# Optimization experiments

Hardware: AMD Instinct MI355X
Metric: run time of the kernel (lower is better)

## Reference

```python
import jax, jax.numpy as jnp
import numpy as np

N, L, S, E, A, D = 16, 256, 128, 128, 9, 768
ARG_ROLES = 23      # score width = ARG_ROLES + 1
MAX_ARG = 9         # hard-coded max_len_arg in the torch module
N_HID = 768


def setup_inputs() -> dict:
    key = jax.random.key(0)
    ks = jax.random.split(key, 10)
    all_embeddings = jax.random.normal(ks[0], (N, L, D), jnp.float32)
    # last-3-layer BERT attention maps, 12 heads, positive entries
    attn_last3 = jax.random.uniform(ks[1], (3, N, 12, L, L), jnp.float32)
    # per-sample sorted distinct first-subword indices (all positive, full length:
    # the ragged filter idxs>0 then keeps everything -> fixed-shape gather)
    idx_keys = jax.random.split(ks[2], N)
    cand = jnp.arange(1, L - MAX_ARG - 1)
    idxs_to_collect = jax.vmap(
        lambda k: jnp.sort(jax.random.choice(k, cand, (S + 2,), replace=False))
    )(idx_keys).astype(jnp.int32)
    is_triggers = (jax.random.uniform(ks[3], (N, S)) < 0.05).astype(jnp.float32)
    is_triggers = is_triggers.at[:, 0].set(1.0)  # >=1 trigger per sample
    entity_mapping = jax.random.normal(ks[4], (N, S, E), jnp.float32) * 0.05
    arg_weight_matrices = jax.random.normal(ks[5], (N, MAX_ARG, A), jnp.float32) * 0.3
    map_keys = jax.random.split(ks[6], N)
    arg_mapping = jax.vmap(
        lambda k: jax.random.permutation(k, ARG_ROLES + 1)[:A]
    )(map_keys).astype(jnp.int32)
    W1 = jax.random.normal(ks[7], (6 * D, N_HID), jnp.float32) * 0.02
    b1 = jnp.zeros((N_HID,), jnp.float32)
    W2 = jax.random.normal(ks[8], (N_HID, 1), jnp.float32) * 0.02
    b2 = jnp.zeros((1,), jnp.float32)
    return {
        "all_embeddings": all_embeddings,
        "attn_last3": attn_last3,
        "entity_mapping": entity_mapping,
        "arg_weight_matrices": arg_weight_matrices,
        "is_triggers": is_triggers,
        "W1": W1, "b1": b1, "W2": W2, "b2": b2,
        "idxs_to_collect": idxs_to_collect,
        "arg_mapping": arg_mapping,
    }


def reference(all_embeddings, attn_last3, entity_mapping, arg_weight_matrices,
              is_triggers, W1, b1, W2, b2, idxs_to_collect, arg_mapping):
    sqrt_d = jnp.sqrt(jnp.asarray(D, jnp.float32))
    sent_idx = idxs_to_collect[:, :S]                      # [N,S] first-subword ids
    # get_fist_subword_embeddings: ragged gather (full-length here)
    sent_emb = jnp.take_along_axis(all_embeddings, sent_idx[:, :, None], axis=1)  # [N,S,D]
    # arg-type tokens sit right after the second-to-last [SEP]
    arg_pos = idxs_to_collect[:, -2:-1] + 1 + jnp.arange(MAX_ARG)[None, :]        # [N,9]
    arg_raw = jnp.take_along_axis(all_embeddings, arg_pos[:, :, None], axis=1)    # [N,9,D]

    entity_emb = jnp.einsum('nsd,nse->ned', sent_emb, entity_mapping)             # [N,E,D]
    trig = jnp.sum(sent_emb * is_triggers[..., None], axis=1) \
           / jnp.sum(is_triggers, axis=1, keepdims=True)                          # [N,D]
    del trig  # _trigger is computed but unused downstream in the torch forward
    arg_emb = jnp.einsum('nkd,nka->nad', arg_raw, arg_weight_matrices)            # [N,A,D]

    # bi-attention scores (broadcast-mul-sum == contraction over D)
    t2a = jnp.einsum('ned,nad->nea', entity_emb, arg_emb) / sqrt_d
    w = (t2a - 5.0) / 2.0                                                         # [N,E,A]
    token_argAwared = jnp.einsum('nea,nad->ned', w, arg_emb)                      # [N,E,D]
    arg_tokenAwared = jnp.einsum('nea,ned->nad', w, entity_emb)                   # [N,A,D]

    # select_hidden_att for each of the last 3 layers
    att_mean = jnp.mean(attn_last3, axis=2)                                       # [3,N,L,L]
    def sel_layer(a):  # a: [N,L,L] -> row/col gather + row renorm
        s = jax.vmap(lambda m, i: m[i][:, i])(a, sent_idx)                        # [N,S,S]
        return s / (jnp.sum(s, axis=-1, keepdims=True) + 1e-9)
    t2t = (sel_layer(att_mean[0]) + sel_layer(att_mean[1]) + sel_layer(att_mean[2])) / 3.0

    h2h_sent = jnp.einsum('nst,ntd->nsd', t2t, sent_emb)                          # [N,S,D]
    # A_h2h and H_ are projected from sent space (S) to entity space (E)
    A_h2h_e = jnp.einsum('nsd,nse->ned', h2h_sent, entity_mapping)                # [N,E,D]
    H_e = entity_emb                                                              # sent_emb projected == entity_emb

    a2a = jax.nn.softmax(jnp.einsum('nad,nbd->nab', arg_emb, arg_emb), axis=-1)   # [N,A,A]
    u2u = jnp.einsum('nab,nbd->nad', a2a, arg_emb)                                # [N,A,D]

    shp = (N, E, A, D)
    H_    = jnp.broadcast_to(H_e[:, :, None, :], shp)
    U_    = jnp.broadcast_to(arg_emb[:, None, :, :], shp)
    A_h2u = jnp.broadcast_to(token_argAwared[:, :, None, :], shp)
    A_h2h = jnp.broadcast_to(A_h2h_e[:, :, None, :], shp)
    A_u2h = jnp.broadcast_to(arg_tokenAwared[:, None, :, :], shp)
    A_u2u = jnp.broadcast_to(u2u[:, None, :, :], shp)
    latent = jnp.concatenate([H_, U_, A_h2u, A_h2h, A_u2h, A_u2u], axis=-1)       # [N,E,A,6D]

    hid = jax.nn.gelu(latent @ W1 + b1, approximate=False)                        # [N,E,A,768]
    score = (hid @ W2 + b2)[..., 0]                                               # [N,E,A]

    # map_arg_to_ids: scatter each arg slot back to its global role id
    def scatter_one(s, ids):  # s [E,A], ids [A]
        return jnp.full((E, ARG_ROLES + 1), -1e6, jnp.float32).at[:, ids].set(s)
    new_score = jax.vmap(scatter_one)(score, arg_mapping)                         # [N,E,24]
    return new_score
```

## Files before the change

### kernel.cpp

```cpp
#include <hip/hip_runtime.h>
#include <math.h>

namespace {
constexpr int N_ = 16, L_ = 256, S_ = 128, E_ = 128, A_ = 9, D_ = 768, H_ = 768, RO_ = 24;
constexpr int IDXW = 130;
constexpr int W1R = 6 * D_;
constexpr float INV_SQRT_D = 0.03608439182435161f;
constexpr int PESZ = 2048 * 768;
constexpr int PASZ = 144 * 768;
constexpr int GB_GATHER = 0;
constexpr int GB_ENTMAP = 192;
constexpr int GB_W1T    = 208;
constexpr int GB_T2T    = 1072;
constexpr int GB_ARGU   = 2096;
constexpr int GB_TOTAL  = 2112;
}

using bshort8 = __attribute__((ext_vector_type(8))) short;
using f32x4v = __attribute__((ext_vector_type(4))) float;

__device__ __forceinline__ unsigned short f2bf(float f) {
    unsigned u = __builtin_bit_cast(unsigned, f);
    return (unsigned short)((u + 0x7fffu + ((u >> 16) & 1u)) >> 16);
}

__global__ __launch_bounds__(256) void stage1_k(const float* __restrict__ all_emb,
                                                const int* __restrict__ idxs,
                                                const float* __restrict__ ent_map,
                                                const float* __restrict__ W1,
                                                const float* __restrict__ argw,
                                                const float* __restrict__ attn,
                                                unsigned short* __restrict__ sentT,
                                                unsigned short* __restrict__ entmapT,
                                                short* __restrict__ W1t,
                                                unsigned short* __restrict__ t2tbf,
                                                float* __restrict__ argE,
                                                unsigned short* __restrict__ argEbf,
                                                unsigned short* __restrict__ u2ubf) {
    __shared__ __align__(16) unsigned char smem[33792];
    const int b = blockIdx.x, tid = threadIdx.x;

    if (b < GB_ENTMAP) {
        const int n = b / 12, d0 = (b % 12) * 64;
        auto tile = (unsigned short (*)[132])smem;
#pragma unroll
        for (int it = 0; it < 8; ++it) {
            const int lin = tid + 256 * it;
            const int s = lin >> 4, dq = (lin & 15) * 4;
            const int row = idxs[n * IDXW + s];
            const float4 v = *reinterpret_cast<const float4*>(all_emb + ((size_t)(n * L_ + row)) * D_ + d0 + dq);
            tile[dq + 0][s] = f2bf(v.x); tile[dq + 1][s] = f2bf(v.y);
            tile[dq + 2][s] = f2bf(v.z); tile[dq + 3][s] = f2bf(v.w);
        }
        __syncthreads();
#pragma unroll
        for (int it = 0; it < 8; ++it) {
            const int lin = tid + 256 * it;
            const int d = lin >> 5, s4 = (lin & 31) * 4;
            ushort4 v = {tile[d][s4], tile[d][s4 + 1], tile[d][s4 + 2], tile[d][s4 + 3]};
            *reinterpret_cast<ushort4*>(sentT + ((size_t)(n * D_) + d0 + d) * S_ + s4) = v;
        }
    } else if (b < GB_W1T) {
        const int n = b - GB_ENTMAP;
        auto tile = (unsigned short (*)[132])smem;
#pragma unroll
        for (int it = 0; it < 16; ++it) {
            const int lin = tid + 256 * it;
            const int s = lin >> 5, eq = (lin & 31) * 4;
            const float4 v = *reinterpret_cast<const float4*>(ent_map + ((size_t)(n * S_ + s)) * E_ + eq);
            tile[eq + 0][s] = f2bf(v.x); tile[eq + 1][s] = f2bf(v.y);
            tile[eq + 2][s] = f2bf(v.z); tile[eq + 3][s] = f2bf(v.w);
        }
        __syncthreads();
#pragma unroll
        for (int it = 0; it < 16; ++it) {
            const int lin = tid + 256 * it;
            const int e = lin >> 5, s4 = (lin & 31) * 4;
            ushort4 v = {tile[e][s4], tile[e][s4 + 1], tile[e][s4 + 2], tile[e][s4 + 3]};
            *reinterpret_cast<ushort4*>(entmapT + ((size_t)(n * E_) + e) * S_ + s4) = v;
        }
    } else if (b < GB_T2T) {
        const int b2 = b - GB_W1T;
        const int k0 = (b2 % 72) * 64, h0 = (b2 / 72) * 64;
        auto tile = (float (*)[65])smem;
        const int tx = tid & 63, ty = tid >> 6;
#pragma unroll
        for (int i = 0; i < 16; ++i) {
            const int r = ty + i * 4;
            tile[r][tx] = W1[(size_t)(k0 + r) * H_ + h0 + tx];
        }
        __syncthreads();
#pragma unroll
        for (int i = 0; i < 16; ++i) {
            const int r = ty + i * 4;
            W1t[(size_t)(h0 + r) * W1R + k0 + tx] = (short)f2bf(tile[tx][r]);
        }
    } else if (b < GB_ARGU) {
        const int idx = b - GB_T2T;
        const int n = idx >> 6;
        const int half = tid >> 7, t128 = tid & 127;
        const int s = ((idx & 63) << 1) | half;
        const int w = t128 >> 6, lane = tid & 63;
        float* sum2 = (float*)smem;
        float* part = (float*)(smem + 12288);
        const int is = idxs[n * IDXW + s], it = idxs[n * IDXW + t128];
#pragma unroll
        for (int l = 0; l < 3; ++l) {
            const float* base = attn + ((size_t)((l * N_ + n) * 12 + w * 6)) * (L_ * L_)
                              + (size_t)is * L_ + lane * 4;
            float4 acc = {0.f, 0.f, 0.f, 0.f};
#pragma unroll
            for (int h = 0; h < 6; ++h) {
// ... 2 lines not shown
            }
            *reinterpret_cast<float4*>(&sum2[(((half * 3 + l) * 2 + w) << 8) + lane * 4]) = acc;
        }
        __syncthreads();
        float m[3];
#pragma unroll
        for (int l = 0; l < 3; ++l) {
            m[l] = (sum2[(((half * 3 + l) * 2 + 0) << 8) + it] +
                    sum2[(((half * 3 + l) * 2 + 1) << 8) + it]) * (1.0f / 12.0f);
            float r = m[l];
#pragma unroll
            for (int off = 32; off; off >>= 1) r += __shfl_xor(r, off, 64);
            if (lane == 0) part[(half * 3 + l) * 2 + w] = r;
        }
        __syncthreads();
        float out = 0.f;
#pragma unroll
        for (int l = 0; l < 3; ++l)
            out += m[l] / (part[(half * 3 + l) * 2 + 0] + part[(half * 3 + l) * 2 + 1] + 1e-9f);
        t2tbf[((size_t)(n * S_ + s)) * S_ + t128] = f2bf(out * (1.0f / 3.0f));
    } else {
        const int n = b - GB_ARGU;
        auto wsm = (float (*)[A_])smem;
        auto part45 = (float (*)[4])(smem + 512);
        auto Psm = (float (*)[A_])(smem + 1536);
        if (tid < A_ * A_) wsm[tid / A_][tid % A_] = argw[n * A_ * A_ + tid];
        __syncthreads();
        const int p0 = idxs[n * IDXW + S_] + 1;
        float pp[45] = {};
        float vals[3][A_];
#pragma unroll
        for (int c = 0; c < 3; ++c) {
            const int d = tid + 256 * c;
            float raw[A_];
#pragma unroll
            for (int k = 0; k < A_; ++k) raw[k] = all_emb[((size_t)(n * L_ + p0 + k)) * D_ + d];
#pragma unroll
            for (int a = 0; a < A_; ++a) {
                float acc = 0.f;
#pragma unroll
                for (int k = 0; k < A_; ++k) acc = fmaf(raw[k], wsm[k][a], acc);
                vals[c][a] = acc;
                argE[((size_t)(n * A_ + a)) * D_ + d] = acc;
                argEbf[((size_t)(n * A_ + a)) * D_ + d] = f2bf(acc);
            }
            int p = 0;
#pragma unroll
            for (int a = 0; a < A_; ++a)
#pragma unroll
                for (int bb = a; bb < A_; ++bb) pp[p++] += vals[c][a] * vals[c][bb];
        }
        const int lane = tid & 63, wv = tid >> 6;
#pragma unroll
        for (int p = 0; p < 45; ++p) {
            float v = pp[p];
            for (int off = 32; off; off >>= 1) v += __shfl_down(v, off, 64);
            if (lane == 0) part45[p][wv] = v;
        }
        __syncthreads();
// ... 4 lines not shown
            float v[A_], mx = -1e30f;
#pragma unroll
            for (int bb = 0; bb < A_; ++bb) {
                const int lo = a < bb ? a : bb, hi = a < bb ? bb : a;
                v[bb] = part45[lo * (19 - lo) / 2 + hi - lo][0];
                mx = fmaxf(mx, v[bb]);
            }
            float sm = 0.f;
#pragma unroll
            for (int bb = 0; bb < A_; ++bb) { v[bb] = expf(v[bb] - mx); sm += v[bb]; }
            const float inv = 1.0f / sm;
#pragma unroll
            for (int bb = 0; bb < A_; ++bb) Psm[a][bb] = v[bb] * inv;
        }
        __syncthreads();
#pragma unroll
        for (int c = 0; c < 3; ++c) {
            const int d = tid + 256 * c;
#pragma unroll
            for (int a = 0; a < A_; ++a) {
                float acc = 0.f;
#pragma unroll
                for (int bb = 0; bb < A_; ++bb) acc = fmaf(Psm[a][bb], vals[c][bb], acc);
                u2ubf[((size_t)(n * A_ + a)) * D_ + d] = f2bf(acc);
            }
        }
    }
}

__global__ __launch_bounds__(256) void gemm_pair_k(const unsigned short* __restrict__ t2tbf,
                                                   const unsigned short* __restrict__ entmapT,
                                                   const unsigned short* __restrict__ sentT,
                                                   float* __restrict__ entf,
                                                   unsigned short* __restrict__ entbf,
                                                   unsigned short* __restrict__ h2hT) {
    __shared__ __align__(16) short As[128][40];
    __shared__ __align__(16) short Bs[64][40];
    const int n = blockIdx.y, c0 = blockIdx.x * 64, z = blockIdx.z;
    const unsigned short* A = (z == 0 ? t2tbf : entmapT) + (size_t)n * S_ * S_;
    const unsigned short* BT = sentT + (size_t)n * D_ * S_;
    const int tid = threadIdx.x;
    const int wave = tid >> 6, lane = tid & 63;
    const int row16 = lane & 15, quad = lane >> 4;
    f32x4v acc[2][4] = {};
    for (int k0 = 0; k0 < S_; k0 += 32) {
#pragma unroll
        for (int i = 0; i < 2; ++i) {
            const int idx = tid + 256 * i;
            const int r = idx >> 2, q = idx & 3;
            *reinterpret_cast<bshort8*>(&As[r][q * 8]) =
                *reinterpret_cast<const bshort8*>(A + (size_t)r * S_ + k0 + q * 8);
        }
        {
            const int col = tid >> 2, q = tid & 3;
            *reinterpret_cast<bshort8*>(&Bs[col][q * 8]) =
                *reinterpret_cast<const bshort8*>(BT + (size_t)(c0 + col) * S_ + k0 + q * 8);
        }
        __syncthreads();
        bshort8 a[2], b[4];
#pragma unroll
        for (int mi = 0; mi < 2; ++mi)
            a[mi] = *reinterpret_cast<const bshort8*>(&As[wave * 32 + mi * 16 + row16][quad * 8]);
#pragma unroll
        for (int ni = 0; ni < 4; ++ni)
            b[ni] = *reinterpret_cast<const bshort8*>(&Bs[ni * 16 + row16][quad * 8]);
#pragma unroll
        for (int mi = 0; mi < 2; ++mi)
#pragma unroll
            for (int ni = 0; ni < 4; ++ni)
                acc[mi][ni] = __builtin_amdgcn_mfma_f32_16x16x32_bf16(a[mi], b[ni], acc[mi][ni], 0, 0, 0);
        __syncthreads();
    }
#pragma unroll
    for (int mi = 0; mi < 2; ++mi) {
#pragma unroll
        for (int ni = 0; ni < 4; ++ni) {
            const int rbase = wave * 32 + mi * 16 + quad * 4;
            const int col = c0 + ni * 16 + row16;
            if (z == 0) {
                ushort4 v = {f2bf(acc[mi][ni][0]), f2bf(acc[mi][ni][1]),
                             f2bf(acc[mi][ni][2]), f2bf(acc[mi][ni][3])};
                *reinterpret_cast<ushort4*>(h2hT + (size_t)n * D_ * S_ + (size_t)col * S_ + rbase) = v;
            } else {
#pragma unroll
                for (int t = 0; t < 4; ++t) {
                    const size_t o = ((size_t)n * S_ + rbase + t) * D_ + col;
                    entf[o] = acc[mi][ni][t];
                    entbf[o] = f2bf(acc[mi][ni][t]);
                }
            }
        }
    }
}

__global__ __launch_bounds__(256) void gemm2_k(const unsigned short* __restrict__ entmapT,
                                               const unsigned short* __restrict__ h2hT,
                                               const unsigned short* __restrict__ entbf,
                                               const unsigned short* __restrict__ argEbf,
                                               unsigned short* __restrict__ Ah2hbf,
                                               float* __restrict__ wbuf) {
    const int bx = blockIdx.x, tid = threadIdx.x;
    const int wave = tid >> 6, lane = tid & 63;
    const int row16 = lane & 15, quad = lane >> 4;
    if (bx < 192) {
        __shared__ __align__(16) short As[128][40];
        __shared__ __align__(16) short Bs[64][40];
        const int n = bx / 12, c0 = (bx % 12) * 64;
        const unsigned short* A = entmapT + (size_t)n * S_ * S_;
        const unsigned short* BT = h2hT + (size_t)n * D_ * S_;
        f32x4v acc[2][4] = {};
        for (int k0 = 0; k0 < S_; k0 += 32) {
#pragma unroll
            for (int i = 0; i < 2; ++i) {
                const int idx = tid + 256 * i;
                const int r = idx >> 2, q = idx & 3;
                *reinterpret_cast<bshort8*>(&As[r][q * 8]) =
                    *reinterpret_cast<const bshort8*>(A + (size_t)r * S_ + k0 + q * 8);
            }
            {
                const int col = tid >> 2, q = tid & 3;
                *reinterpret_cast<bshort8*>(&Bs[col][q * 8]) =
                    *reinterpret_cast<const bshort8*>(BT + (size_t)(c0 + col) * S_ + k0 + q * 8);
            }
            __syncthreads();
            bshort8 a[2], b[4];
#pragma unroll
            for (int mi = 0; mi < 2; ++mi)
                a[mi] = *reinterpret_cast<const bshort8*>(&As[wave * 32 + mi * 16 + row16][quad * 8]);
#pragma unroll
            for (int ni = 0; ni < 4; ++ni)
                b[ni] = *reinterpret_cast<const bshort8*>(&Bs[ni * 16 + row16][quad * 8]);
#pragma unroll
            for (int mi = 0; mi < 2; ++mi)
#pragma unroll
                for (int ni = 0; ni < 4; ++ni)
                    acc[mi][ni] = __builtin_amdgcn_mfma_f32_16x16x32_bf16(a[mi], b[ni], acc[mi][ni], 0, 0, 0);
            __syncthreads();
        }
#pragma unroll
        for (int mi = 0; mi < 2; ++mi)
#pragma unroll
            for (int ni = 0; ni < 4; ++ni) {
                const int rbase = wave * 32 + mi * 16 + quad * 4;
                const int col = c0 + ni * 16 + row16;
#pragma unroll
                for (int t = 0; t < 4; ++t)
                    Ah2hbf[((size_t)n * S_ + rbase + t) * D_ + col] = f2bf(acc[mi][ni][t]);
            }
    } else {
        const int n = bx - 192;
        const unsigned short* Aent = entbf + (size_t)n * E_ * D_;
        const unsigned short* Barg = argEbf + (size_t)n * A_ * D_;
        f32x4v acc[2] = {};
        for (int k0 = 0; k0 < D_; k0 += 32) {
            bshort8 a[2], b;
#pragma unroll
            for (int mi = 0; mi < 2; ++mi)
                a[mi] = *reinterpret_cast<const bshort8*>(Aent + (size_t)(wave * 32 + mi * 16 + row16) * D_ + k0 + quad * 8);
            b = *reinterpret_cast<const bshort8*>(Barg + (size_t)row16 * D_ + k0 + quad * 8);
#pragma unroll
            for (int mi = 0; mi < 2; ++mi)
                acc[mi] = __builtin_amdgcn_mfma_f32_16x16x32_bf16(a[mi], b, acc[mi], 0, 0, 0);
        }
        if (row16 < A_) {
#pragma unroll
            for (int mi = 0; mi < 2; ++mi)
#pragma unroll
                for (int t = 0; t < 4; ++t) {
                    const int e = wave * 32 + mi * 16 + quad * 4 + t;
                    const float w = (acc[mi][t] * INV_SQRT_D - 5.0f) * 0.5f;
                    wbuf[((size_t)(n * E_ + e)) * A_ + row16] = w;
                }
        }
    }
}

__global__ __launch_bounds__(256) void post_k(const float* __restrict__ wbuf,
                                              const float* __restrict__ argE,
                                              const float* __restrict__ entf,
                                              unsigned short* __restrict__ tokAbf,
                                              unsigned short* __restrict__ argTbf) {
    const int b = blockIdx.x, tid = threadIdx.x;
    if (b < N_ * E_) {
        const int n = b >> 7, e = b & 127;
        __shared__ float wl[A_];
        if (tid < A_) wl[tid] = wbuf[(size_t)(n * E_ + e) * A_ + tid];
        __syncthreads();
        const float* ar = argE + (size_t)n * A_ * D_;
#pragma unroll
        for (int c = 0; c < 3; ++c) {
            const int d = tid + 256 * c;
            float s = 0.f;
#pragma unroll
            for (int a = 0; a < A_; ++a) s = fmaf(wl[a], ar[(size_t)a * D_ + d], s);
            tokAbf[((size_t)(n * E_ + e)) * D_ + d] = f2bf(s);
        }
    } else {
        const int idx = b - N_ * E_;
        const int n = idx / A_, a = idx % A_;
        __shared__ float wl[E_];
        if (tid < E_) wl[tid] = wbuf[(size_t)(n * E_ + tid) * A_ + a];
        __syncthreads();
        const float* eb = entf + (size_t)n * E_ * D_;
#pragma unroll
        for (int c = 0; c < 3; ++c) {
            const int d = tid + 256 * c;
            float acc = 0.f;
            for (int e = 0; e < E_; ++e) acc = fmaf(wl[e], eb[(size_t)e * D_ + d], acc);
            argTbf[((size_t)(n * A_ + a)) * D_ + d] = f2bf(acc);
        }
    }
}

__global__ __launch_bounds__(256) void mfma_mlp_k(const unsigned short* __restrict__ e0,
                                                  const unsigned short* __restrict__ e1,
                                                  const unsigned short* __restrict__ e2,
                                                  const unsigned short* __restrict__ a0,
                                                  const unsigned short* __restrict__ a1,
                                                  const unsigned short* __restrict__ a2,
                                                  const short* __restrict__ W1t,
                                                  float* __restrict__ Pe3, float* __restrict__ Pa3) {
    __shared__ __align__(16) short As[128][40];
    __shared__ __align__(16) short Bs[64][40];
    const int bx = blockIdx.x;
    const int seg = bx % 3;
    const int blk = bx / 3;
    const bool isPa = blk >= 16;
    const unsigned short* Aseg;
    int woff;
    if (isPa) {
        Aseg = seg == 0 ? a0 : (seg == 1 ? a1 : a2);
        woff = seg == 0 ? 1 * D_ : (seg == 1 ? 4 * D_ : 5 * D_);
    } else {
        Aseg = seg == 0 ? e0 : (seg == 1 ? e1 : e2);
        woff = seg == 0 ? 0 : (seg == 1 ? 2 * D_ : 3 * D_);
    }
    const int M = isPa ? N_ * A_ : N_ * E_;
    const int r0 = (isPa ? blk - 16 : blk) * 128;
    float* C = isPa ? (Pa3 + (size_t)seg * PASZ) : (Pe3 + (size_t)seg * PESZ);
    const int c0 = blockIdx.y * 64;
    const int tid = threadIdx.x;
    const int wave = tid >> 6, lane = tid & 63;
    const int row16 = lane & 15, quad = lane >> 4;
    f32x4v acc[2][4] = {};
    for (int kk = 0; kk < D_; kk += 32) {
#pragma unroll
        for (int i = 0; i < 2; ++i) {
            const int idx = tid + 256 * i;
            const int r = idx >> 2, q = idx & 3;
            bshort8 av = {};
            if (r0 + r < M) av = *reinterpret_cast<const bshort8*>(Aseg + (size_t)(r0 + r) * D_ + kk + q * 8);
            *reinterpret_cast<bshort8*>(&As[r][q * 8]) = av;
        }
        {
            const int col = tid >> 2, q = tid & 3;
            *reinterpret_cast<bshort8*>(&Bs[col][q * 8]) =
                *reinterpret_cast<const bshort8*>(W1t + (size_t)(c0 + col) * W1R + woff + kk + q * 8);
        }
        __syncthreads();
        bshort8 a[2], b[4];
#pragma unroll
        for (int mi = 0; mi < 2; ++mi)
            a[mi] = *reinterpret_cast<const bshort8*>(&As[wave * 32 + mi * 16 + row16][quad * 8]);
#pragma unroll
        for (int ni = 0; ni < 4; ++ni)
            b[ni] = *reinterpret_cast<const bshort8*>(&Bs[ni * 16 + row16][quad * 8]);
#pragma unroll
        for (int mi = 0; mi < 2; ++mi)
#pragma unroll
            for (int ni = 0; ni < 4; ++ni)
                acc[mi][ni] = __builtin_amdgcn_mfma_f32_16x16x32_bf16(a[mi], b[ni], acc[mi][ni], 0, 0, 0);
        __syncthreads();
    }
#pragma unroll
    for (int mi = 0; mi < 2; ++mi) {
#pragma unroll
        for (int ni = 0; ni < 4; ++ni) {
            const int rbase = r0 + wave * 32 + mi * 16 + quad * 4;
            const int col = c0 + ni * 16 + row16;
#pragma unroll
            for (int t = 0; t < 4; ++t)
                if (rbase + t < M) C[(size_t)(rbase + t) * H_ + col] = acc[mi][ni][t];
        }
    }
}

__global__ __launch_bounds__(256) void score_k(const float* __restrict__ Pe3, const float* __restrict__ Pa3,
                                               const float* __restrict__ b1, const float* __restrict__ W2,
                                               const float* __restrict__ b2, const int* __restrict__ arg_map,
                                               float* __restrict__ out) {
    const int n = blockIdx.x >> 7, e = blockIdx.x & 127;
    const int tid = threadIdx.x;
    __shared__ float paS[A_ * H_];
    __shared__ float part[A_][4];
    float* orow = out + ((size_t)(n * E_ + e)) * RO_;
    if (tid < RO_) orow[tid] = -1000000.0f;
    for (int i = tid; i < A_ * H_; i += 256) {
        const size_t o = (size_t)n * A_ * H_ + i;
        paS[i] = Pa3[o] + Pa3[PASZ + o] + Pa3[2 * PASZ + o];
    }
    __syncthreads();
    const size_t ro = ((size_t)(n * E_ + e)) * H_;
    float acc[A_] = {};
    for (int h = tid; h < H_; h += 256) {
        const float pe = Pe3[ro + h] + Pe3[PESZ + ro + h] + Pe3[2 * PESZ + ro + h] + b1[h];
        const float w2 = W2[h];
#pragma unroll
        for (int a = 0; a < A_; ++a) {
            const float x = pe + paS[a * H_ + h];
            const float g = x * 0.5f * (1.0f + erff(x * 0.70710678118654752f));
            acc[a] = fmaf(g, w2, acc[a]);
        }
    }
    const int lane = tid & 63, wv = tid >> 6;
#pragma unroll
    for (int a = 0; a < A_; ++a)
        for (int off = 32; off; off >>= 1) acc[a] += __shfl_down(acc[a], off, 64);
    if (lane == 0)
        for (int a = 0; a < A_; ++a) part[a][wv] = acc[a];
    __syncthreads();
// ... 7 lines not shown
                              void* d_out, int out_size, void* d_ws, size_t ws_size,
                              hipStream_t stream) {
    const float* all_emb = (const float*)d_in[0];
    const float* attn    = (const float*)d_in[1];
    const float* ent_map = (const float*)d_in[2];
    const float* argw    = (const float*)d_in[3];
    const float* W1 = (const float*)d_in[5];
    const float* b1 = (const float*)d_in[6];
    const float* W2 = (const float*)d_in[7];
    const float* b2 = (const float*)d_in[8];
    const int* idxs    = (const int*)d_in[9];
    const int* arg_map = (const int*)d_in[10];
    float* out = (float*)d_out;

    float* ws = (float*)d_ws;
    float* entf = ws + 0;
    float* Pe3  = ws + 1572864;
    float* argE = ws + 6291456;
    float* wbuf = ws + 6402048;
    float* Pa3  = ws + 6420480;
    short*          W1t     = (short*)(ws + 6752256);
    unsigned short* sentT   = (unsigned short*)(ws + 8521728);
    unsigned short* entmapT = (unsigned short*)(ws + 9308160);
    unsigned short* t2tbf   = (unsigned short*)(ws + 9439232);
    unsigned short* argEbf  = (unsigned short*)(ws + 9570304);
    unsigned short* u2ubf   = (unsigned short*)(ws + 9625600);
    unsigned short* entbf   = (unsigned short*)(ws + 9680896);
    unsigned short* h2hT    = (unsigned short*)(ws + 10467328);
    unsigned short* Ah2hbf  = (unsigned short*)(ws + 11253760);
    unsigned short* tokAbf  = (unsigned short*)(ws + 12040192);
    unsigned short* argTbf  = (unsigned short*)(ws + 12826624);

    stage1_k<<<GB_TOTAL, 256, 0, stream>>>(all_emb, idxs, ent_map, W1, argw, attn,
                                           sentT, entmapT, W1t, t2tbf, argE, argEbf, u2ubf);

    gemm_pair_k<<<dim3(D_ / 64, N_, 2), 256, 0, stream>>>(t2tbf, entmapT, sentT, entf, entbf, h2hT);

    gemm2_k<<<208, 256, 0, stream>>>(entmapT, h2hT, entbf, argEbf, Ah2hbf, wbuf);

    post_k<<<N_ * E_ + N_ * A_, 256, 0, stream>>>(wbuf, argE, entf, tokAbf, argTbf);

    mfma_mlp_k<<<dim3(54, H_ / 64), 256, 0, stream>>>(entbf, tokAbf, Ah2hbf, argEbf, argTbf, u2ubf, W1t, Pe3, Pa3);

    score_k<<<N_ * E_, 256, 0, stream>>>(Pe3, Pa3, b1, W2, b2, arg_map, out);

    (void)in_sizes; (void)n_in; (void)out_size; (void)ws_size;
}
```

Before: 318.2 us.

## Reassociate MLP first layer through W1 to shrink the GEMM chain

Restructures the pipeline so the embedding gather is multiplied by W1 slices first, and the entity, attention and softmax mixing matrices are then applied to the already projected 768-wide products. The separate entity, h2h, token-aware and u2u intermediates and their split-K partial outputs go away, and the six-kernel chain becomes five kernels with fused partial sums. The aim is to cut GEMM work and intermediate memory traffic. In exchange, more bf16 rounding points sit in a different order, and the kernels have more complex block-index dispatch.

```diff
diff --git a/kernel.cpp b/kernel.cpp
--- a/kernel.cpp
+++ b/kernel.cpp
@@ -6,14 +6,12 @@
 constexpr int IDXW = 130;
 constexpr int W1R = 6 * D_;
 constexpr float INV_SQRT_D = 0.03608439182435161f;
-constexpr int PESZ = 2048 * 768;
-constexpr int PASZ = 144 * 768;
-constexpr int GB_GATHER = 0;
-constexpr int GB_ENTMAP = 192;
-constexpr int GB_W1T    = 208;
-constexpr int GB_T2T    = 1072;
-constexpr int GB_ARGU   = 2096;
-constexpr int GB_TOTAL  = 2112;
+constexpr int GB_T2T    = 0;
+constexpr int GB_W1T    = 1024;
+constexpr int GB_GATHER = 1888;
+constexpr int GB_ENTMAP = 1952;
+constexpr int GB_ARGU   = 1968;
+constexpr int GB_TOTAL  = 1984;
 }
 
 using bshort8 = __attribute__((ext_vector_type(8))) short;
@@ -22,6 +20,46 @@
 __device__ __forceinline__ unsigned short f2bf(float f) {
     unsigned u = __builtin_bit_cast(unsigned, f);
     return (unsigned short)((u + 0x7fffu + ((u >> 16) & 1u)) >> 16);
+}
+__device__ __forceinline__ float bf2f(unsigned short u) {
+    return __builtin_bit_cast(float, ((unsigned)u) << 16);
+}
+
+__device__ __forceinline__ void gemm_tileK(const unsigned short* __restrict__ A, int lda,
+                                           const unsigned short* __restrict__ BT, int ldb,
+                                           int klen, int c0, int tid,
+                                           short (*As)[40], short (*Bs)[40],
+                                           f32x4v acc[2][4]) {
+    const int wave = tid >> 6, lane = tid & 63;
+    const int row16 = lane & 15, quad = lane >> 4;
+    for (int k0 = 0; k0 < klen; k0 += 32) {
+#pragma unroll
+        for (int i = 0; i < 2; ++i) {
+            const int idx = tid + 256 * i;
+            const int r = idx >> 2, q = idx & 3;
+            *reinterpret_cast<bshort8*>(&As[r][q * 8]) =
+                *reinterpret_cast<const bshort8*>(A + (size_t)r * lda + k0 + q * 8);
+        }
+        {
+            const int col = tid >> 2, q = tid & 3;
+            *reinterpret_cast<bshort8*>(&Bs[col][q * 8]) =
+                *reinterpret_cast<const bshort8*>(BT + (size_t)(c0 + col) * ldb + k0 + q * 8);
+        }
+        __syncthreads();
+        bshort8 a[2], b[4];
+#pragma unroll
+        for (int mi = 0; mi < 2; ++mi)
+            a[mi] = *reinterpret_cast<const bshort8*>(&As[wave * 32 + mi * 16 + row16][quad * 8]);
+#pragma unroll
+        for (int ni = 0; ni < 4; ++ni)
+            b[ni] = *reinterpret_cast<const bshort8*>(&Bs[ni * 16 + row16][quad * 8]);
+#pragma unroll
+        for (int mi = 0; mi < 2; ++mi)
+#pragma unroll
+            for (int ni = 0; ni < 4; ++ni)
+                acc[mi][ni] = __builtin_amdgcn_mfma_f32_16x16x32_bf16(a[mi], b[ni], acc[mi][ni], 0, 0, 0);
+        __syncthreads();
+    }
 }
 
 __global__ __launch_bounds__(256) void stage1_k(const float* __restrict__ all_emb,
@@ -30,72 +68,16 @@
                                                 const float* __restrict__ W1,
                                                 const float* __restrict__ argw,
                                                 const float* __restrict__ attn,
-                                                unsigned short* __restrict__ sentT,
+                                                unsigned short* __restrict__ sentbf,
                                                 unsigned short* __restrict__ entmapT,
                                                 short* __restrict__ W1t,
                                                 unsigned short* __restrict__ t2tbf,
-                                                float* __restrict__ argE,
                                                 unsigned short* __restrict__ argEbf,
-                                                unsigned short* __restrict__ u2ubf) {
+                                                float* __restrict__ Pmat) {
     __shared__ __align__(16) unsigned char smem[33792];
     const int b = blockIdx.x, tid = threadIdx.x;
 
-    if (b < GB_ENTMAP) {
-        const int n = b / 12, d0 = (b % 12) * 64;
-        auto tile = (unsigned short (*)[132])smem;
-#pragma unroll
-        for (int it = 0; it < 8; ++it) {
-            const int lin = tid + 256 * it;
-            const int s = lin >> 4, dq = (lin & 15) * 4;
-            const int row = idxs[n * IDXW + s];
-            const float4 v = *reinterpret_cast<const float4*>(all_emb + ((size_t)(n * L_ + row)) * D_ + d0 + dq);
-            tile[dq + 0][s] = f2bf(v.x); tile[dq + 1][s] = f2bf(v.y);
-            tile[dq + 2][s] = f2bf(v.z); tile[dq + 3][s] = f2bf(v.w);
-        }
-        __syncthreads();
-#pragma unroll
-        for (int it = 0; it < 8; ++it) {
-            const int lin = tid + 256 * it;
-            const int d = lin >> 5, s4 = (lin & 31) * 4;
-            ushort4 v = {tile[d][s4], tile[d][s4 + 1], tile[d][s4 + 2], tile[d][s4 + 3]};
-            *reinterpret_cast<ushort4*>(sentT + ((size_t)(n * D_) + d0 + d) * S_ + s4) = v;
-        }
-    } else if (b < GB_W1T) {
-        const int n = b - GB_ENTMAP;
-        auto tile = (unsigned short (*)[132])smem;
-#pragma unroll
-        for (int it = 0; it < 16; ++it) {
-            const int lin = tid + 256 * it;
-            const int s = lin >> 5, eq = (lin & 31) * 4;
-            const float4 v = *reinterpret_cast<const float4*>(ent_map + ((size_t)(n * S_ + s)) * E_ + eq);
-            tile[eq + 0][s] = f2bf(v.x); tile[eq + 1][s] = f2bf(v.y);
-            tile[eq + 2][s] = f2bf(v.z); tile[eq + 3][s] = f2bf(v.w);
-        }
-        __syncthreads();
-#pragma unroll
-        for (int it = 0; it < 16; ++it) {
-            const int lin = tid + 256 * it;
-            const int e = lin >> 5, s4 = (lin & 31) * 4;
-            ushort4 v = {tile[e][s4], tile[e][s4 + 1], tile[e][s4 + 2], tile[e][s4 + 3]};
-            *reinterpret_cast<ushort4*>(entmapT + ((size_t)(n * E_) + e) * S_ + s4) = v;
-        }
-    } else if (b < GB_T2T) {
-        const int b2 = b - GB_W1T;
-        const int k0 = (b2 % 72) * 64, h0 = (b2 / 72) * 64;
-        auto tile = (float (*)[65])smem;
-        const int tx = tid & 63, ty = tid >> 6;
-#pragma unroll
-        for (int i = 0; i < 16; ++i) {
-            const int r = ty + i * 4;
-            tile[r][tx] = W1[(size_t)(k0 + r) * H_ + h0 + tx];
-        }
-        __syncthreads();
-#pragma unroll
-        for (int i = 0; i < 16; ++i) {
-            const int r = ty + i * 4;
-            W1t[(size_t)(h0 + r) * W1R + k0 + tx] = (short)f2bf(tile[tx][r]);
-        }
-    } else if (b < GB_ARGU) {
+    if (b < GB_W1T) {
         const int idx = b - GB_T2T;
         const int n = idx >> 6;
         const int half = tid >> 7, t128 = tid & 127;
@@ -128,17 +110,65 @@
             if (lane == 0) part[(half * 3 + l) * 2 + w] = r;
         }
         __syncthreads();
-        float out = 0.f;
+        float o = 0.f;
 #pragma unroll
         for (int l = 0; l < 3; ++l)
-            out += m[l] / (part[(half * 3 + l) * 2 + 0] + part[(half * 3 + l) * 2 + 1] + 1e-9f);
-        t2tbf[((size_t)(n * S_ + s)) * S_ + t128] = f2bf(out * (1.0f / 3.0f));
+            o += m[l] / (part[(half * 3 + l) * 2 + 0] + part[(half * 3 + l) * 2 + 1] + 1e-9f);
+        t2tbf[((size_t)(n * S_ + s)) * S_ + t128] = f2bf(o * (1.0f / 3.0f));
+    } else if (b < GB_GATHER) {
+        const int b2 = b - GB_W1T;
+        const int k0 = (b2 % 72) * 64, h0 = (b2 / 72) * 64;
+        auto tile = (float (*)[65])smem;
+        const int tx = tid & 63, ty = tid >> 6;
+#pragma unroll
+        for (int i = 0; i < 16; ++i) {
+            const int r = ty + i * 4;
+            tile[r][tx] = W1[(size_t)(k0 + r) * H_ + h0 + tx];
+        }
+        __syncthreads();
+#pragma unroll
+        for (int i = 0; i < 16; ++i) {
+            const int r = ty + i * 4;
+            W1t[(size_t)(h0 + r) * W1R + k0 + tx] = (short)f2bf(tile[tx][r]);
+        }
+    } else if (b < GB_ENTMAP) {
+        const int b2 = b - GB_GATHER;
+        const int n = b2 >> 2, r0 = (b2 & 3) * 32;
+#pragma unroll
+        for (int it = 0; it < 24; ++it) {
+            const int lin = tid + 256 * it;
+            const int row = lin / 192, dq = (lin % 192) * 4;
+            const int grow = idxs[n * IDXW + r0 + row];
+            const float4 v = *reinterpret_cast<const float4*>(all_emb + ((size_t)(n * L_ + grow)) * D_ + dq);
+            ushort4 u = {f2bf(v.x), f2bf(v.y), f2bf(v.z), f2bf(v.w)};
+            *reinterpret_cast<ushort4*>(sentbf + ((size_t)(n * S_) + r0 + row) * D_ + dq) = u;
+        }
+    } else if (b < GB_ARGU) {
+        const int n = b - GB_ENTMAP;
+        auto tile = (unsigned short (*)[132])smem;
+#pragma unroll
+        for (int it = 0; it < 16; ++it) {
+            const int lin = tid + 256 * it;
+            const int s = lin >> 5, eq = (lin & 31) * 4;
+            const float4 v = *reinterpret_cast<const float4*>(ent_map + ((size_t)(n * S_ + s)) * E_ + eq);
+            tile[eq + 0][s] = f2bf(v.x); tile[eq + 1][s] = f2bf(v.y);
+            tile[eq + 2][s] = f2bf(v.z); tile[eq + 3][s] = f2bf(v.w);
+        }
+        __syncthreads();
+#pragma unroll
+        for (int it = 0; it < 16; ++it) {
+            const int lin = tid + 256 * it;
+            const int e = lin >> 5, s4 = (lin & 31) * 4;
+            ushort4 v = {tile[e][s4], tile[e][s4 + 1], tile[e][s4 + 2], tile[e][s4 + 3]};
+            *reinterpret_cast<ushort4*>(entmapT + ((size_t)(n * E_) + e) * S_ + s4) = v;
+        }
     } else {
         const int n = b - GB_ARGU;
         auto wsm = (float (*)[A_])smem;
         auto part45 = (float (*)[4])(smem + 512);
         auto Psm = (float (*)[A_])(smem + 1536);
         if (tid < A_ * A_) wsm[tid / A_][tid % A_] = argw[n * A_ * A_ + tid];
+        for (int i = tid; i < 7 * D_; i += 256) argEbf[((size_t)(n * 16) + 9) * D_ + i] = 0;
         __syncthreads();
         const int p0 = idxs[n * IDXW + S_] + 1;
         float pp[45] = {};
@@ -155,8 +185,7 @@
 #pragma unroll
                 for (int k = 0; k < A_; ++k) acc = fmaf(raw[k], wsm[k][a], acc);
                 vals[c][a] = acc;
-                argE[((size_t)(n * A_ + a)) * D_ + d] = acc;
-                argEbf[((size_t)(n * A_ + a)) * D_ + d] = f2bf(acc);
+                argEbf[((size_t)(n * 16 + a)) * D_ + d] = f2bf(acc);
             }
             int p = 0;
 #pragma unroll
@@ -191,100 +220,178 @@
             for (int bb = 0; bb < A_; ++bb) Psm[a][bb] = v[bb] * inv;
         }
         __syncthreads();
-#pragma unroll
-        for (int c = 0; c < 3; ++c) {
-            const int d = tid + 256 * c;
-#pragma unroll
-            for (int a = 0; a < A_; ++a) {
-                float acc = 0.f;
-#pragma unroll
-                for (int bb = 0; bb < A_; ++bb) acc = fmaf(Psm[a][bb], vals[c][bb], acc);
-                u2ubf[((size_t)(n * A_ + a)) * D_ + d] = f2bf(acc);
-            }
-        }
-    }
-}
-
-__global__ __launch_bounds__(256) void gemm_pair_k(const unsigned short* __restrict__ t2tbf,
-                                                   const unsigned short* __restrict__ entmapT,
-                                                   const unsigned short* __restrict__ sentT,
-                                                   float* __restrict__ entf,
-                                                   unsigned short* __restrict__ entbf,
-                                                   unsigned short* __restrict__ h2hT) {
+        if (tid < A_ * A_) Pmat[n * 81 + tid] = Psm[tid / A_][tid % A_];
+    }
+}
+
+__global__ __launch_bounds__(256) void l2_k(const unsigned short* __restrict__ sentbf,
+                                            const short* __restrict__ W1t,
+                                            const unsigned short* __restrict__ argEbf,
+                                            unsigned short* __restrict__ SWT,
+                                            float* __restrict__ argEW,
+                                            unsigned short* __restrict__ SAT) {
     __shared__ __align__(16) short As[128][40];
     __shared__ __align__(16) short Bs[64][40];
-    const int n = blockIdx.y, c0 = blockIdx.x * 64, z = blockIdx.z;
-    const unsigned short* A = (z == 0 ? t2tbf : entmapT) + (size_t)n * S_ * S_;
-    const unsigned short* BT = sentT + (size_t)n * D_ * S_;
-    const int tid = threadIdx.x;
+    const int bx = blockIdx.x, tid = threadIdx.x;
     const int wave = tid >> 6, lane = tid & 63;
     const int row16 = lane & 15, quad = lane >> 4;
-    f32x4v acc[2][4] = {};
-    for (int k0 = 0; k0 < S_; k0 += 32) {
-#pragma unroll
-        for (int i = 0; i < 2; ++i) {
-            const int idx = tid + 256 * i;
-            const int r = idx >> 2, q = idx & 3;
-            *reinterpret_cast<bshort8*>(&As[r][q * 8]) =
-                *reinterpret_cast<const bshort8*>(A + (size_t)r * S_ + k0 + q * 8);
-        }
-        {
-            const int col = tid >> 2, q = tid & 3;
-            *reinterpret_cast<bshort8*>(&Bs[col][q * 8]) =
-                *reinterpret_cast<const bshort8*>(BT + (size_t)(c0 + col) * S_ + k0 + q * 8);
-        }
-        __syncthreads();
-        bshort8 a[2], b[4];
+    if (bx < 576) {
+        const int j3 = bx / 192;
+        const int jseg = (j3 == 0 ? 0 : (j3 == 1 ? 3 : 4));
+        const int rem = bx % 192;
+        const int n = rem / 12, c0 = (rem % 12) * 64;
+        f32x4v acc[2][4] = {};
+        gemm_tileK(sentbf + (size_t)n * S_ * D_, D_,
+                   (const unsigned short*)W1t + (size_t)jseg * D_, W1R,
+                   D_, c0, tid, As, Bs, acc);
+        unsigned short* outb = SWT + ((size_t)(j3 * N_ + n)) * H_ * S_;
 #pragma unroll
         for (int mi = 0; mi < 2; ++mi)
-            a[mi] = *reinterpret_cast<const bshort8*>(&As[wave * 32 + mi * 16 + row16][quad * 8]);
-#pragma unroll
-        for (int ni = 0; ni < 4; ++ni)
-            b[ni] = *reinterpret_cast<const bshort8*>(&Bs[ni * 16 + row16][quad * 8]);
-#pragma unroll
-        for (int mi = 0; mi < 2; ++mi)
-#pragma unroll
-            for (int ni = 0; ni < 4; ++ni)
-                acc[mi][ni] = __builtin_amdgcn_mfma_f32_16x16x32_bf16(a[mi], b[ni], acc[mi][ni], 0, 0, 0);
-        __syncthreads();
-    }
-#pragma unroll
-    for (int mi = 0; mi < 2; ++mi) {
-#pragma unroll
-        for (int ni = 0; ni < 4; ++ni) {
-            const int rbase = wave * 32 + mi * 16 + quad * 4;
-            const int col = c0 + ni * 16 + row16;
-            if (z == 0) {
+#pragma unroll
+            for (int ni = 0; ni < 4; ++ni) {
+                const int rbase = wave * 32 + mi * 16 + quad * 4;
+                const int col = c0 + ni * 16 + row16;
                 ushort4 v = {f2bf(acc[mi][ni][0]), f2bf(acc[mi][ni][1]),
                              f2bf(acc[mi][ni][2]), f2bf(acc[mi][ni][3])};
-                *reinterpret_cast<ushort4*>(h2hT + (size_t)n * D_ * S_ + (size_t)col * S_ + rbase) = v;
-            } else {
-#pragma unroll
-                for (int t = 0; t < 4; ++t) {
-                    const size_t o = ((size_t)n * S_ + rbase + t) * D_ + col;
-                    entf[o] = acc[mi][ni][t];
-                    entbf[o] = f2bf(acc[mi][ni][t]);
-                }
-            }
-        }
-    }
-}
-
-__global__ __launch_bounds__(256) void gemm2_k(const unsigned short* __restrict__ entmapT,
-                                               const unsigned short* __restrict__ h2hT,
-                                               const unsigned short* __restrict__ entbf,
-                                               const unsigned short* __restrict__ argEbf,
-                                               unsigned short* __restrict__ Ah2hbf,
-                                               float* __restrict__ wbuf) {
+                *reinterpret_cast<ushort4*>(outb + (size_t)col * S_ + rbase) = v;
+            }
+    } else if (bx < 624) {
+        const int idx = bx - 576;
+        const int j3 = idx / 16;
+        const int jseg = (j3 == 0 ? 1 : (j3 == 1 ? 2 : 5));
+        const int n = idx % 16;
+        const unsigned short* Ar = argEbf + (size_t)n * 16 * D_;
+        const unsigned short* BT = (const unsigned short*)W1t + (size_t)jseg * D_;
+        float* outp = argEW + ((size_t)(j3 * N_ + n)) * A_ * H_;
+#pragma unroll
+        for (int i = 0; i < 12; ++i) {
+            const int col0 = (wave * 12 + i) * 16;
+            f32x4v acc = {};
+            for (int k0 = 0; k0 < D_; k0 += 32) {
+                bshort8 a8 = *reinterpret_cast<const bshort8*>(Ar + (size_t)row16 * D_ + k0 + quad * 8);
+                bshort8 b8 = *reinterpret_cast<const bshort8*>(BT + (size_t)(col0 + row16) * W1R + k0 + quad * 8);
+                acc = __builtin_amdgcn_mfma_f32_16x16x32_bf16(a8, b8, acc, 0, 0, 0);
+            }
+#pragma unroll
+            for (int t = 0; t < 4; ++t) {
+                const int a = quad * 4 + t;
+                if (a < A_) outp[(size_t)a * H_ + col0 + row16] = acc[t];
+            }
+        }
+    } else {
+        const int n = bx - 624;
+        const unsigned short* Asent = sentbf + (size_t)n * S_ * D_;
+        const unsigned short* BT = argEbf + (size_t)n * 16 * D_;
+        f32x4v acc[2] = {};
+        for (int k0 = 0; k0 < D_; k0 += 32) {
+            bshort8 a8[2], b8;
+#pragma unroll
+            for (int mi = 0; mi < 2; ++mi)
+                a8[mi] = *reinterpret_cast<const bshort8*>(Asent + (size_t)(wave * 32 + mi * 16 + row16) * D_ + k0 + quad * 8);
+            b8 = *reinterpret_cast<const bshort8*>(BT + (size_t)row16 * D_ + k0 + quad * 8);
+#pragma unroll
+            for (int mi = 0; mi < 2; ++mi)
+                acc[mi] = __builtin_amdgcn_mfma_f32_16x16x32_bf16(a8[mi], b8, acc[mi], 0, 0, 0);
+        }
+#pragma unroll
+        for (int mi = 0; mi < 2; ++mi) {
+            const int rbase = wave * 32 + mi * 16 + quad * 4;
+            ushort4 v = {f2bf(acc[mi][0]), f2bf(acc[mi][1]), f2bf(acc[mi][2]), f2bf(acc[mi][3])};
+            *reinterpret_cast<ushort4*>(SAT + ((size_t)(n * 16) + row16) * S_ + rbase) = v;
+        }
+    }
+}
+
+__global__ __launch_bounds__(256) void l3_k(const unsigned short* __restrict__ t2tbf,
+                                            const unsigned short* __restrict__ entmapT,
+                                            const unsigned short* __restrict__ SWT,
+                                            const unsigned short* __restrict__ SAT,
+                                            unsigned short* __restrict__ T3T,
+                                            unsigned short* __restrict__ EW4T,
+                                            float* __restrict__ wfp,
+                                            unsigned short* __restrict__ wTbf) {
+    __shared__ __align__(16) short As[128][40];
+    __shared__ __align__(16) short Bs[64][40];
+    const int bx = blockIdx.x, tid = threadIdx.x;
+    const int wave = tid >> 6, lane = tid & 63;
+    const int row16 = lane & 15, quad = lane >> 4;
+    if (bx < 384) {
+        const int z = bx / 192;
+        const int idx = bx % 192;
+        const int n = idx / 12, c0 = (idx % 12) * 64;
+        const unsigned short* A = (z == 0 ? t2tbf : entmapT) + (size_t)n * S_ * S_;
+        const unsigned short* BT = SWT + ((size_t)((z + 1) * N_ + n)) * H_ * S_;
+        unsigned short* outb = (z == 0 ? T3T : EW4T) + (size_t)n * H_ * S_;
+        f32x4v acc[2][4] = {};
+        gemm_tileK(A, S_, BT, S_, S_, c0, tid, As, Bs, acc);
+#pragma unroll
+        for (int mi = 0; mi < 2; ++mi)
+#pragma unroll
+            for (int ni = 0; ni < 4; ++ni) {
+                const int rbase = wave * 32 + mi * 16 + quad * 4;
+                const int col = c0 + ni * 16 + row16;
+                ushort4 v = {f2bf(acc[mi][ni][0]), f2bf(acc[mi][ni][1]),
+                             f2bf(acc[mi][ni][2]), f2bf(acc[mi][ni][3])};
+                *reinterpret_cast<ushort4*>(outb + (size_t)col * S_ + rbase) = v;
+            }
+    } else {
+        const int n = bx - 384;
+        const unsigned short* A = entmapT + (size_t)n * S_ * S_;
+        const unsigned short* BT = SAT + (size_t)n * 16 * S_;
+        f32x4v acc[2] = {};
+        for (int k0 = 0; k0 < S_; k0 += 32) {
+            bshort8 a8[2], b8;
+#pragma unroll
+            for (int mi = 0; mi < 2; ++mi)
+                a8[mi] = *reinterpret_cast<const bshort8*>(A + (size_t)(wave * 32 + mi * 16 + row16) * S_ + k0 + quad * 8);
+            b8 = *reinterpret_cast<const bshort8*>(BT + (size_t)row16 * S_ + k0 + quad * 8);
+#pragma unroll
+            for (int mi = 0; mi < 2; ++mi)
+                acc[mi] = __builtin_amdgcn_mfma_f32_16x16x32_bf16(a8[mi], b8, acc[mi], 0, 0, 0);
+        }
+#pragma unroll
+        for (int mi = 0; mi < 2; ++mi) {
+            const int rbase = wave * 32 + mi * 16 + quad * 4;
+            float wv[4];
+            ushort4 u;
+#pragma unroll
+            for (int t = 0; t < 4; ++t) {
+                wv[t] = (acc[mi][t] * INV_SQRT_D - 5.0f) * 0.5f;
+                if (row16 < A_) wfp[((size_t)(n * E_) + rbase + t) * A_ + row16] = wv[t];
+            }
+            u.x = f2bf(wv[0]); u.y = f2bf(wv[1]); u.z = f2bf(wv[2]); u.w = f2bf(wv[3]);
+            *reinterpret_cast<ushort4*>(wTbf + ((size_t)(n * 16) + row16) * S_ + rbase) = u;
+        }
+    }
+}
+
+__global__ __launch_bounds__(256) void l4_k(const unsigned short* __restrict__ entmapT,
+                                            const unsigned short* __restrict__ SWT,
+                                            const unsigned short* __restrict__ T3T,
+                                            const float* __restrict__ wfp,
+                                            const float* __restrict__ argEW,
+                                            const unsigned short* __restrict__ wTbf,
+                                            const unsigned short* __restrict__ EW4T,
+                                            const float* __restrict__ Pmat,
+                                            float* __restrict__ Pe, float* __restrict__ Pa) {
+    __shared__ __align__(16) unsigned char smem[28416];
     const int bx = blockIdx.x, tid = threadIdx.x;
     const int wave = tid >> 6, lane = tid & 63;
     const int row16 = lane & 15, quad = lane >> 4;
     if (bx < 192) {
-        __shared__ __align__(16) short As[128][40];
-        __shared__ __align__(16) short Bs[64][40];
+        short (*As)[40] = (short (*)[40])smem;
+        short (*Bs)[40] = (short (*)[40])(smem + 10240);
+        float* wS = (float*)(smem + 15360);
+        float* aW2 = (float*)(smem + 19968);
         const int n = bx / 12, c0 = (bx % 12) * 64;
+        for (int i = tid; i < E_ * A_; i += 256) wS[i] = wfp[(size_t)n * E_ * A_ + i];
+        for (int i = tid; i < A_ * 64; i += 256) {
+            const int a = i >> 6, hc = i & 63;
+            aW2[i] = argEW[((size_t)(1 * N_ + n) * A_ + a) * H_ + c0 + hc];
+        }
         const unsigned short* A = entmapT + (size_t)n * S_ * S_;
-        const unsigned short* BT = h2hT + (size_t)n * D_ * S_;
+        const unsigned short* B0 = SWT + ((size_t)(0 * N_ + n)) * H_ * S_;
+        const unsigned short* B1 = T3T + (size_t)n * H_ * S_;
         f32x4v acc[2][4] = {};
         for (int k0 = 0; k0 < S_; k0 += 32) {
 #pragma unroll
@@ -296,8 +403,13 @@
             }
             {
                 const int col = tid >> 2, q = tid & 3;
-                *reinterpret_cast<bshort8*>(&Bs[col][q * 8]) =
-                    *reinterpret_cast<const bshort8*>(BT + (size_t)(c0 + col) * S_ + k0 + q * 8);
+                const bshort8 u0 = *reinterpret_cast<const bshort8*>(B0 + (size_t)(c0 + col) * S_ + k0 + q * 8);
+                const bshort8 u1 = *reinterpret_cast<const bshort8*>(B1 + (size_t)(c0 + col) * S_ + k0 + q * 8);
+                bshort8 s;
+#pragma unroll
+                for (int e8 = 0; e8 < 8; ++e8)
+                    s[e8] = (short)f2bf(bf2f((unsigned short)u0[e8]) + bf2f((unsigned short)u1[e8]));
+                *reinterpret_cast<bshort8*>(&Bs[col][q * 8]) = s;
             }
             __syncthreads();
             bshort8 a[2], b[4];
@@ -319,150 +431,51 @@
 #pragma unroll
             for (int ni = 0; ni < 4; ++ni) {
                 const int rbase = wave * 32 + mi * 16 + quad * 4;
-                const int col = c0 + ni * 16 + row16;
-#pragma unroll
-                for (int t = 0; t < 4; ++t)
-                    Ah2hbf[((size_t)n * S_ + rbase + t) * D_ + col] = f2bf(acc[mi][ni][t]);
+                const int hc = ni * 16 + row16;
+#pragma unroll
+                for (int t = 0; t < 4; ++t) {
+                    const int e = rbase + t;
+                    float v = acc[mi][ni][t];
+#pragma unroll
+                    for (int a = 0; a < A_; ++a) v = fmaf(wS[e * A_ + a], aW2[a * 64 + hc], v);
+                    Pe[((size_t)(n * E_) + e) * H_ + c0 + hc] = v;
+                }
             }
     } else {
         const int n = bx - 192;
-        const unsigned short* Aent = entbf + (size_t)n * E_ * D_;
-        const unsigned short* Barg = argEbf + (size_t)n * A_ * D_;
-        f32x4v acc[2] = {};
-        for (int k0 = 0; k0 < D_; k0 += 32) {
-            bshort8 a[2], b;
-#pragma unroll
-            for (int mi = 0; mi < 2; ++mi)
-                a[mi] = *reinterpret_cast<const bshort8*>(Aent + (size_t)(wave * 32 + mi * 16 + row16) * D_ + k0 + quad * 8);
-            b = *reinterpret_cast<const bshort8*>(Barg + (size_t)row16 * D_ + k0 + quad * 8);
-#pragma unroll
-            for (int mi = 0; mi < 2; ++mi)
-                acc[mi] = __builtin_amdgcn_mfma_f32_16x16x32_bf16(a[mi], b, acc[mi], 0, 0, 0);
-        }
-        if (row16 < A_) {
-#pragma unroll
-            for (int mi = 0; mi < 2; ++mi)
-#pragma unroll
-                for (int t = 0; t < 4; ++t) {
-                    const int e = wave * 32 + mi * 16 + quad * 4 + t;
-                    const float w = (acc[mi][t] * INV_SQRT_D - 5.0f) * 0.5f;
-                    wbuf[((size_t)(n * E_ + e)) * A_ + row16] = w;
+        float* a5 = (float*)smem;
+        float* Pm = (float*)(smem + 27648);
+        for (int i = tid; i < A_ * H_; i += 256) a5[i] = argEW[((size_t)(2 * N_ + n)) * A_ * H_ + i];
+        if (tid < A_ * A_) Pm[tid] = Pmat[n * 81 + tid];
+        __syncthreads();
+        const unsigned short* A = wTbf + (size_t)n * 16 * S_;
+        const unsigned short* BT = EW4T + (size_t)n * H_ * S_;
+        const float* a1 = argEW + ((size_t)(0 * N_ + n)) * A_ * H_;
+#pragma unroll
+        for (int i = 0; i < 12; ++i) {
+            const int col0 = (wave * 12 + i) * 16;
+            f32x4v acc = {};
+            for (int k0 = 0; k0 < S_; k0 += 32) {
+                bshort8 a8 = *reinterpret_cast<const bshort8*>(A + (size_t)row16 * S_ + k0 + quad * 8);
+                bshort8 b8 = *reinterpret_cast<const bshort8*>(BT + (size_t)(col0 + row16) * S_ + k0 + quad * 8);
+                acc = __builtin_amdgcn_mfma_f32_16x16x32_bf16(a8, b8, acc, 0, 0, 0);
+            }
+            const int h = col0 + row16;
+#pragma unroll
+            for (int t = 0; t < 4; ++t) {
+                const int a = quad * 4 + t;
+                if (a < A_) {
+                    float v = acc[t] + a1[(size_t)a * H_ + h];
+#pragma unroll
+                    for (int bb = 0; bb < A_; ++bb) v = fmaf(Pm[a * A_ + bb], a5[bb * H_ + h], v);
+                    Pa[((size_t)(n * A_) + a) * H_ + h] = v;
                 }
-        }
-    }
-}
-
-__global__ __launch_bounds__(256) void post_k(const float* __restrict__ wbuf,
-                                              const float* __restrict__ argE,
-                                              const float* __restrict__ entf,
-                                              unsigned short* __restrict__ tokAbf,
-                                              unsigned short* __restrict__ argTbf) {
-    const int b = blockIdx.x, tid = threadIdx.x;
-    if (b < N_ * E_) {
-        const int n = b >> 7, e = b & 127;
-        __shared__ float wl[A_];
-        if (tid < A_) wl[tid] = wbuf[(size_t)(n * E_ + e) * A_ + tid];
-        __syncthreads();
-        const float* ar = argE + (size_t)n * A_ * D_;
-#pragma unroll
-        for (int c = 0; c < 3; ++c) {
-            const int d = tid + 256 * c;
-            float s = 0.f;
-#pragma unroll
-            for (int a = 0; a < A_; ++a) s = fmaf(wl[a], ar[(size_t)a * D_ + d], s);
-            tokAbf[((size_t)(n * E_ + e)) * D_ + d] = f2bf(s);
-        }
-    } else {
-        const int idx = b - N_ * E_;
-        const int n = idx / A_, a = idx % A_;
-        __shared__ float wl[E_];
-        if (tid < E_) wl[tid] = wbuf[(size_t)(n * E_ + tid) * A_ + a];
-        __syncthreads();
-        const float* eb = entf + (size_t)n * E_ * D_;
-#pragma unroll
-        for (int c = 0; c < 3; ++c) {
-            const int d = tid + 256 * c;
-            float acc = 0.f;
-            for (int e = 0; e < E_; ++e) acc = fmaf(wl[e], eb[(size_t)e * D_ + d], acc);
-            argTbf[((size_t)(n * A_ + a)) * D_ + d] = f2bf(acc);
-        }
-    }
-}
-
-__global__ __launch_bounds__(256) void mfma_mlp_k(const unsigned short* __restrict__ e0,
-                                                  const unsigned short* __restrict__ e1,
-                                                  const unsigned short* __restrict__ e2,
-                                                  const unsigned short* __restrict__ a0,
-                                                  const unsigned short* __restrict__ a1,
-                                                  const unsigned short* __restrict__ a2,
-                                                  const short* __restrict__ W1t,
-                                                  float* __restrict__ Pe3, float* __restrict__ Pa3) {
-    __shared__ __align__(16) short As[128][40];
-    __shared__ __align__(16) short Bs[64][40];
-    const int bx = blockIdx.x;
-    const int seg = bx % 3;
-    const int blk = bx / 3;
-    const bool isPa = blk >= 16;
-    const unsigned short* Aseg;
-    int woff;
-    if (isPa) {
-        Aseg = seg == 0 ? a0 : (seg == 1 ? a1 : a2);
-        woff = seg == 0 ? 1 * D_ : (seg == 1 ? 4 * D_ : 5 * D_);
-    } else {
-        Aseg = seg == 0 ? e0 : (seg == 1 ? e1 : e2);
-        woff = seg == 0 ? 0 : (seg == 1 ? 2 * D_ : 3 * D_);
-    }
-    const int M = isPa ? N_ * A_ : N_ * E_;
-    const int r0 = (isPa ? blk - 16 : blk) * 128;
-    float* C = isPa ? (Pa3 + (size_t)seg * PASZ) : (Pe3 + (size_t)seg * PESZ);
-    const int c0 = blockIdx.y * 64;
-    const int tid = threadIdx.x;
-    const int wave = tid >> 6, lane = tid & 63;
-    const int row16 = lane & 15, quad = lane >> 4;
-    f32x4v acc[2][4] = {};
-    for (int kk = 0; kk < D_; kk += 32) {
-#pragma unroll
-        for (int i = 0; i < 2; ++i) {
-            const int idx = tid + 256 * i;
-            const int r = idx >> 2, q = idx & 3;
-            bshort8 av = {};
-            if (r0 + r < M) av = *reinterpret_cast<const bshort8*>(Aseg + (size_t)(r0 + r) * D_ + kk + q * 8);
-            *reinterpret_cast<bshort8*>(&As[r][q * 8]) = av;
-        }
-        {
-            const int col = tid >> 2, q = tid & 3;
-            *reinterpret_cast<bshort8*>(&Bs[col][q * 8]) =
-                *reinterpret_cast<const bshort8*>(W1t + (size_t)(c0 + col) * W1R + woff + kk + q * 8);
-        }
-        __syncthreads();
-        bshort8 a[2], b[4];
-#pragma unroll
-        for (int mi = 0; mi < 2; ++mi)
-            a[mi] = *reinterpret_cast<const bshort8*>(&As[wave * 32 + mi * 16 + row16][quad * 8]);
-#pragma unroll
-        for (int ni = 0; ni < 4; ++ni)
-            b[ni] = *reinterpret_cast<const bshort8*>(&Bs[ni * 16 + row16][quad * 8]);
-#pragma unroll
-        for (int mi = 0; mi < 2; ++mi)
-#pragma unroll
-            for (int ni = 0; ni < 4; ++ni)
-                acc[mi][ni] = __builtin_amdgcn_mfma_f32_16x16x32_bf16(a[mi], b[ni], acc[mi][ni], 0, 0, 0);
-        __syncthreads();
-    }
-#pragma unroll
-    for (int mi = 0; mi < 2; ++mi) {
-#pragma unroll
-        for (int ni = 0; ni < 4; ++ni) {
-            const int rbase = r0 + wave * 32 + mi * 16 + quad * 4;
-            const int col = c0 + ni * 16 + row16;
-#pragma unroll
-            for (int t = 0; t < 4; ++t)
-                if (rbase + t < M) C[(size_t)(rbase + t) * H_ + col] = acc[mi][ni][t];
-        }
-    }
-}
-
-__global__ __launch_bounds__(256) void score_k(const float* __restrict__ Pe3, const float* __restrict__ Pa3,
+            }
+        }
+    }
+}
+
+__global__ __launch_bounds__(256) void score_k(const float* __restrict__ Pe, const float* __restrict__ Pa,
                                                const float* __restrict__ b1, const float* __restrict__ W2,
                                                const float* __restrict__ b2, const int* __restrict__ arg_map,
                                                float* __restrict__ out) {
@@ -472,15 +485,12 @@
     __shared__ float part[A_][4];
     float* orow = out + ((size_t)(n * E_ + e)) * RO_;
     if (tid < RO_) orow[tid] = -1000000.0f;
-    for (int i = tid; i < A_ * H_; i += 256) {
-        const size_t o = (size_t)n * A_ * H_ + i;
-        paS[i] = Pa3[o] + Pa3[PASZ + o] + Pa3[2 * PASZ + o];
-    }
+    for (int i = tid; i < A_ * H_; i += 256) paS[i] = Pa[(size_t)n * A_ * H_ + i];
     __syncthreads();
     const size_t ro = ((size_t)(n * E_ + e)) * H_;
     float acc[A_] = {};
     for (int h = tid; h < H_; h += 256) {
-        const float pe = Pe3[ro + h] + Pe3[PESZ + ro + h] + Pe3[2 * PESZ + ro + h] + b1[h];
+        const float pe = Pe[ro + h] + b1[h];
         const float w2 = W2[h];
 #pragma unroll
         for (int a = 0; a < A_; ++a) {
@@ -518,35 +528,28 @@
     float* out = (float*)d_out;
 
     float* ws = (float*)d_ws;
-    float* entf = ws + 0;
-    float* Pe3  = ws + 1572864;
-    float* argE = ws + 6291456;
-    float* wbuf = ws + 6402048;
-    float* Pa3  = ws + 6420480;
-    short*          W1t     = (short*)(ws + 6752256);
-    unsigned short* sentT   = (unsigned short*)(ws + 8521728);
-    unsigned short* entmapT = (unsigned short*)(ws + 9308160);
-    unsigned short* t2tbf   = (unsigned short*)(ws + 9439232);
-    unsigned short* argEbf  = (unsigned short*)(ws + 9570304);
-    unsigned short* u2ubf   = (unsigned short*)(ws + 9625600);
-    unsigned short* entbf   = (unsigned short*)(ws + 9680896);
-    unsigned short* h2hT    = (unsigned short*)(ws + 10467328);
-    unsigned short* Ah2hbf  = (unsigned short*)(ws + 11253760);
-    unsigned short* tokAbf  = (unsigned short*)(ws + 12040192);
-    unsigned short* argTbf  = (unsigned short*)(ws + 12826624);
+    float* Pe    = ws + 0;
+    float* Pa    = ws + 1572864;
+    float* wfp   = ws + 1683456;
+    float* argEW = ws + 1701888;
+    float* Pmat  = ws + 2033664;
+    short*          W1t     = (short*)(ws + 2034960);
+    unsigned short* sentbf  = (unsigned short*)(ws + 3804432);
+    unsigned short* entmapT = (unsigned short*)(ws + 4590864);
+    unsigned short* t2tbf   = (unsigned short*)(ws + 4721936);
+    unsigned short* argEbf  = (unsigned short*)(ws + 4853008);
+    unsigned short* SWT     = (unsigned short*)(ws + 4951312);
+    unsigned short* SAT     = (unsigned short*)(ws + 7310608);
+    unsigned short* T3T     = (unsigned short*)(ws + 7326992);
+    unsigned short* EW4T    = (unsigned short*)(ws + 8113424);
+    unsigned short* wTbf    = (unsigned short*)(ws + 8899856);
 
     stage1_k<<<GB_TOTAL, 256, 0, stream>>>(all_emb, idxs, ent_map, W1, argw, attn,
-                                           sentT, entmapT, W1t, t2tbf, argE, argEbf, u2ubf);
-
-    gemm_pair_k<<<dim3(D_ / 64, N_, 2), 256, 0, stream>>>(t2tbf, entmapT, sentT, entf, entbf, h2hT);
-
-    gemm2_k<<<208, 256, 0, stream>>>(entmapT, h2hT, entbf, argEbf, Ah2hbf, wbuf);
-
-    post_k<<<N_ * E_ + N_ * A_, 256, 0, stream>>>(wbuf, argE, entf, tokAbf, argTbf);
-
-    mfma_mlp_k<<<dim3(54, H_ / 64), 256, 0, stream>>>(entbf, tokAbf, Ah2hbf, argEbf, argTbf, u2ubf, W1t, Pe3, Pa3);
-
-    score_k<<<N_ * E_, 256, 0, stream>>>(Pe3, Pa3, b1, W2, b2, arg_map, out);
+                                           sentbf, entmapT, W1t, t2tbf, argEbf, Pmat);
+    l2_k<<<640, 256, 0, stream>>>(sentbf, W1t, argEbf, SWT, argEW, SAT);
+    l3_k<<<400, 256, 0, stream>>>(t2tbf, entmapT, SWT, SAT, T3T, EW4T, wfp, wTbf);
+    l4_k<<<208, 256, 0, stream>>>(entmapT, SWT, T3T, wfp, argEW, wTbf, EW4T, Pmat, Pe, Pa);
+    score_k<<<N_ * E_, 256, 0, stream>>>(Pe, Pa, b1, W2, b2, arg_map, out);
 
     (void)in_sizes; (void)n_in; (void)out_size; (void)ws_size;
 }
```

Result: slower. 359.1 us (+12.8%).
